# Kernel tuning notes

Measured on AMD Instinct MI355X. Metric: run time of the kernel, lower is better.

Reference implementation:

```python
import jax, jax.numpy as jnp
import numpy as np

BN_EPS = 1e-5


def setup_inputs() -> dict:
    key = jax.random.key(0)
    k1, k2, k3, k4, k5 = jax.random.split(key, 5)
    B, M, N = 4, 65536, 16384
    C_pre, C_cur, D_out = 64, 128, 128
    C_in = C_pre + C_cur  # 192
    pre_x = jax.random.normal(k1, (B, C_pre, M), dtype=jnp.float32)
    cur_x = jax.random.normal(k2, (B, C_cur, N), dtype=jnp.float32)
    up_idx = jax.random.randint(k3, (B, M, 1), 0, N, dtype=jnp.int64)
    w = jax.random.normal(k4, (C_in, D_out), dtype=jnp.float32) * 0.05
    b = jax.random.normal(k5, (D_out,), dtype=jnp.float32) * 0.05
    gamma = jnp.ones((D_out,), dtype=jnp.float32)
    beta = jnp.zeros((D_out,), dtype=jnp.float32)
    run_mean = jnp.zeros((D_out,), dtype=jnp.float32)
    run_var = jnp.ones((D_out,), dtype=jnp.float32)
    return {"pre_x": pre_x, "cur_x": cur_x, "up_idx": up_idx, "w": w, "b": b,
            "gamma": gamma, "beta": beta, "run_mean": run_mean, "run_var": run_var}


def reference(pre_x, cur_x, up_idx, w, b, gamma, beta, run_mean, run_var):
    # indexing_neighbor(cur_x.permute(0,2,1), up_idx).squeeze(2):
    # gather coarse-point features at nearest-neighbor indices -> [B, C_cur, M]
    idx = up_idx[:, :, 0]                                   # [B, M]
    feat = jnp.take_along_axis(cur_x, idx[:, None, :], axis=2)  # [B, C_cur, M]
    x = jnp.concatenate([pre_x, feat], axis=1)              # [B, C_in, M]
    # ConvTranspose1d(kernel=1) == pointwise linear with weight [C_in, D_out]
    y = jnp.einsum('bcm,cd->bdm', x, w) + b[None, :, None]  # [B, D_out, M]
    # BatchNorm1d (inference form with running stats) + ReLU
    inv = jax.lax.rsqrt(run_var + BN_EPS)
    y = (y - run_mean[None, :, None]) * (inv * gamma)[None, :, None] + beta[None, :, None]
    y = jnp.maximum(y, 0.0)
    return y.transpose(0, 2, 1)                             # [B, M, D_out]
```

## Files before the change

### kernel.cpp

```cpp
#include <hip/hip_runtime.h>
#include <hip/hip_bf16.h>


typedef short bhalf8 __attribute__((ext_vector_type(8)));
typedef float f32x4 __attribute__((ext_vector_type(4)));
typedef unsigned int u32x4 __attribute__((ext_vector_type(4)));

__device__ __forceinline__ short f2bf(float f) {
  unsigned int u = __float_as_uint(f);
  unsigned int r = (u + 0x7fffu + ((u >> 16) & 1u)) >> 16;
  return (short)r;
}

__global__ __launch_bounds__(256) void transpose_cur(const float* __restrict__ cur,
                                                     short* __restrict__ curT) {
  __shared__ float tile[128][65];
  const int b = blockIdx.y;
  const int n0 = blockIdx.x << 6;
  const float* src = cur + (size_t)b * 128 * 16384;
#pragma unroll
  for (int it = 0; it < 8; ++it) {
    int v = it * 256 + threadIdx.x;
    int cc = v >> 4;
    int nq = (v & 15) << 2;
    f32x4 f = __builtin_nontemporal_load(
        reinterpret_cast<const f32x4*>(&src[(size_t)cc * 16384 + n0 + nq]));
    tile[cc][nq + 0] = f[0];
    tile[cc][nq + 1] = f[1];
    tile[cc][nq + 2] = f[2];
    tile[cc][nq + 3] = f[3];
  }
  __syncthreads();
  short* dst = curT + ((size_t)b * 16384 + n0) * 128;
#pragma unroll
  for (int it = 0; it < 4; ++it) {
    int v = it * 256 + threadIdx.x;
    int nn = v >> 4;
    int c8 = (v & 15) << 3;
    bhalf8 pk;
#pragma unroll
    for (int j = 0; j < 8; ++j) pk[j] = f2bf(tile[c8 + j][nn]);
    *reinterpret_cast<bhalf8*>(&dst[(size_t)nn * 128 + c8]) = pk;
  }
}

#define NBLK 2048

__global__ __launch_bounds__(256, 3) void fused_gemm(
    const float* __restrict__ pre_x,
    const int* __restrict__ up_idx,
    const float* __restrict__ w,
    const float* __restrict__ bias,
    const float* __restrict__ gamma, const float* __restrict__ beta,
    const float* __restrict__ rmean, const float* __restrict__ rvar,
    const short* __restrict__ curT,
    float* __restrict__ out)
{
  __shared__ short x_lds[64 * 200];
  const int tid = threadIdx.x;
  const int lane = tid & 63;
  const int wv = tid >> 6;
  const int c = lane & 15;
  const int g = lane >> 4;

  bhalf8 bf[6][2];
#pragma unroll
  for (int s = 0; s < 6; ++s)
#pragma unroll
    for (int ct = 0; ct < 2; ++ct) {
      const int col = 32 * wv + 16 * ct + c;
#pragma unroll
      for (int j = 0; j < 8; ++j)
        bf[s][ct][j] = f2bf(w[(32 * s + 8 * g + j) * 128 + col]);
    }

  float scale[2], shift[2];
#pragma unroll
  for (int ct = 0; ct < 2; ++ct) {
    const int d = 32 * wv + 16 * ct + c;
    float sc = gamma[d] * rsqrtf(rvar[d] + 1e-5f);
    scale[ct] = sc;
    shift[ct] = (bias[d] - rmean[d]) * sc + beta[d];
  }

  for (int t = 0; t < 2; ++t) {
    const long rg = blockIdx.x + (long)t * NBLK;
    const long r0 = rg << 6;
    const int b = (int)(r0 >> 16);
    const int m0 = (int)(r0 & 65535);
    if (t) __syncthreads();

    {
      const float* pb = pre_x + (size_t)b * 64 * 65536 + m0;
#pragma unroll
      for (int it = 0; it < 4; ++it) {
        int v = it * 256 + tid;
        int cc = v >> 4;
        int mq = (v & 15) << 2;
        f32x4 f = __builtin_nontemporal_load(
            reinterpret_cast<const f32x4*>(&pb[(size_t)cc * 65536 + mq]));
        x_lds[(mq + 0) * 200 + cc] = f2bf(f[0]);
        x_lds[(mq + 1) * 200 + cc] = f2bf(f[1]);
        x_lds[(mq + 2) * 200 + cc] = f2bf(f[2]);
        x_lds[(mq + 3) * 200 + cc] = f2bf(f[3]);
      }
    }
    {
#pragma unroll
      for (int it = 0; it < 4; ++it) {
        int mm = it * 16 + (tid >> 4);
        int seg = tid & 15;
        int n = up_idx[r0 + mm];
        const short* srcp = curT + ((size_t)b * 16384 + n) * 128 + seg * 8;
        *reinterpret_cast<u32x4*>(&x_lds[mm * 200 + 64 + seg * 8]) =
            *reinterpret_cast<const u32x4*>(srcp);
      }
    }
    __syncthreads();

#pragma unroll
    for (int rt = 0; rt < 4; ++rt) {
      bhalf8 a[6];
#pragma unroll
      for (int s = 0; s < 6; ++s)
        a[s] = *reinterpret_cast<const bhalf8*>(
            &x_lds[(16 * rt + c) * 200 + 32 * s + 8 * g]);
      f32x4 acc0 = {0.f, 0.f, 0.f, 0.f};
      f32x4 acc1 = {0.f, 0.f, 0.f, 0.f};
#pragma unroll
      for (int s = 0; s < 6; ++s) {
        acc0 = __builtin_amdgcn_mfma_f32_16x16x32_bf16(a[s], bf[s][0], acc0, 0, 0, 0);
        acc1 = __builtin_amdgcn_mfma_f32_16x16x32_bf16(a[s], bf[s][1], acc1, 0, 0, 0);
      }
      float* ob = out + (size_t)(r0 + 16 * rt + 4 * g) * 128 + 32 * wv;
#pragma unroll
      for (int i = 0; i < 4; ++i) {
        float v0 = fmaxf(acc0[i] * scale[0] + shift[0], 0.f);
        float v1 = fmaxf(acc1[i] * scale[1] + shift[1], 0.f);
        __builtin_nontemporal_store(v0, ob + (size_t)i * 128 + c);
        __builtin_nontemporal_store(v1, ob + (size_t)i * 128 + 16 + c);
      }
    }
  }
}

extern "C" void kernel_launch(void* const* d_in, const int* in_sizes, int n_in,
                              void* d_out, int out_size, void* d_ws, size_t ws_size,
                              hipStream_t stream) {
  const float* pre_x = (const float*)d_in[0];
  const float* cur_x = (const float*)d_in[1];
  const int* up_idx = (const int*)d_in[2];
  const float* w = (const float*)d_in[3];
  const float* bias = (const float*)d_in[4];
  const float* gamma = (const float*)d_in[5];
  const float* beta = (const float*)d_in[6];
  const float* rmean = (const float*)d_in[7];
  const float* rvar = (const float*)d_in[8];
  float* out = (float*)d_out;
  short* curT = (short*)d_ws;

  hipLaunchKernelGGL(transpose_cur, dim3(256, 4), dim3(256), 0, stream, cur_x, curT);
  hipLaunchKernelGGL(fused_gemm, dim3(NBLK), dim3(256), 0, stream, pre_x, up_idx, w,
                     bias, gamma, beta, rmean, rvar, curT, out);
}
```

Before: 237.7 us.

## Precompute cur_x projection before gather to shrink main GEMM K

The cur_x half of the weight is now applied to the coarse points first (a GEMM over 16384 points per batch that writes bf16 projections Z), and the main kernel gathers projected rows from Z instead of raw features. This works because a gather commutes with a pointwise linear map. The main kernel's K dimension drops from 192 to 64, which cuts MFMA work, register use and LDS size, and occupancy is raised to 4. In exchange the projection is rounded to bf16 before the pre_x contribution is added, and the first kernel now does a small GEMM instead of only transposing.

```diff
diff --git a/kernel.cpp b/kernel.cpp
--- a/kernel.cpp
+++ b/kernel.cpp
@@ -11,69 +11,113 @@
   unsigned int r = (u + 0x7fffu + ((u >> 16) & 1u)) >> 16;
   return (short)r;
 }
-
-__global__ __launch_bounds__(256) void transpose_cur(const float* __restrict__ cur,
-                                                     short* __restrict__ curT) {
-  __shared__ float tile[128][65];
-  const int b = blockIdx.y;
-  const int n0 = blockIdx.x << 6;
-  const float* src = cur + (size_t)b * 128 * 16384;
-#pragma unroll
-  for (int it = 0; it < 8; ++it) {
-    int v = it * 256 + threadIdx.x;
-    int cc = v >> 4;
-    int nq = (v & 15) << 2;
-    f32x4 f = __builtin_nontemporal_load(
-        reinterpret_cast<const f32x4*>(&src[(size_t)cc * 16384 + n0 + nq]));
-    tile[cc][nq + 0] = f[0];
-    tile[cc][nq + 1] = f[1];
-    tile[cc][nq + 2] = f[2];
-    tile[cc][nq + 3] = f[3];
-  }
-  __syncthreads();
-  short* dst = curT + ((size_t)b * 16384 + n0) * 128;
-#pragma unroll
-  for (int it = 0; it < 4; ++it) {
-    int v = it * 256 + threadIdx.x;
-    int nn = v >> 4;
-    int c8 = (v & 15) << 3;
-    bhalf8 pk;
-#pragma unroll
-    for (int j = 0; j < 8; ++j) pk[j] = f2bf(tile[c8 + j][nn]);
-    *reinterpret_cast<bhalf8*>(&dst[(size_t)nn * 128 + c8]) = pk;
-  }
-}
-
-#define NBLK 2048
-
-__global__ __launch_bounds__(256, 3) void fused_gemm(
-    const float* __restrict__ pre_x,
-    const int* __restrict__ up_idx,
-    const float* __restrict__ w,
-    const float* __restrict__ bias,
-    const float* __restrict__ gamma, const float* __restrict__ beta,
-    const float* __restrict__ rmean, const float* __restrict__ rvar,
-    const short* __restrict__ curT,
-    float* __restrict__ out)
-{
-  __shared__ short x_lds[64 * 200];
+__device__ __forceinline__ float bf2f(short s) {
+  return __uint_as_float(((unsigned int)(unsigned short)s) << 16);
+}
+
+#define ZST 136
+#define PST 72
+
+__global__ __launch_bounds__(256, 4) void cur_gemm(const float* __restrict__ cur,
+                                                   const float* __restrict__ w,
+                                                   short* __restrict__ Z) {
+  __shared__ short lds[64 * ZST];
   const int tid = threadIdx.x;
   const int lane = tid & 63;
   const int wv = tid >> 6;
   const int c = lane & 15;
   const int g = lane >> 4;
-
-  bhalf8 bf[6][2];
-#pragma unroll
-  for (int s = 0; s < 6; ++s)
+  const int r0 = blockIdx.x << 6;
+  const int b = r0 >> 14;
+  const int n0 = r0 & 16383;
+  const float* src = cur + (size_t)b * 128 * 16384 + n0;
+
+  bhalf8 bw[4][2];
+#pragma unroll
+  for (int s = 0; s < 4; ++s)
 #pragma unroll
     for (int ct = 0; ct < 2; ++ct) {
       const int col = 32 * wv + 16 * ct + c;
 #pragma unroll
       for (int j = 0; j < 8; ++j)
-        bf[s][ct][j] = f2bf(w[(32 * s + 8 * g + j) * 128 + col]);
-    }
-
+        bw[s][ct][j] = f2bf(w[(64 + 32 * s + 8 * g + j) * 128 + col]);
+    }
+
+#pragma unroll
+  for (int it = 0; it < 8; ++it) {
+    int v = it * 256 + tid;
+    int cc = v >> 4;
+    int nq = (v & 15) << 2;
+    f32x4 f = __builtin_nontemporal_load(
+        reinterpret_cast<const f32x4*>(&src[(size_t)cc * 16384 + nq]));
+#pragma unroll
+    for (int k = 0; k < 4; ++k) lds[(nq + k) * ZST + cc] = f2bf(f[k]);
+  }
+  __syncthreads();
+
+  f32x4 acc[4][2];
+#pragma unroll
+  for (int rt = 0; rt < 4; ++rt) {
+    bhalf8 a[4];
+#pragma unroll
+    for (int s = 0; s < 4; ++s)
+      a[s] = *reinterpret_cast<const bhalf8*>(&lds[(16 * rt + c) * ZST + 32 * s + 8 * g]);
+    acc[rt][0] = (f32x4){0.f, 0.f, 0.f, 0.f};
+    acc[rt][1] = (f32x4){0.f, 0.f, 0.f, 0.f};
+#pragma unroll
+    for (int s = 0; s < 4; ++s) {
+      acc[rt][0] = __builtin_amdgcn_mfma_f32_16x16x32_bf16(a[s], bw[s][0], acc[rt][0], 0, 0, 0);
+      acc[rt][1] = __builtin_amdgcn_mfma_f32_16x16x32_bf16(a[s], bw[s][1], acc[rt][1], 0, 0, 0);
+    }
+  }
+  __syncthreads();
+#pragma unroll
+  for (int rt = 0; rt < 4; ++rt)
+#pragma unroll
+    for (int ct = 0; ct < 2; ++ct)
+#pragma unroll
+      for (int i = 0; i < 4; ++i)
+        lds[(16 * rt + 4 * g + i) * ZST + 32 * wv + 16 * ct + c] = f2bf(acc[rt][ct][i]);
+  __syncthreads();
+  short* dst = Z + (size_t)r0 * 128;
+  const int row = tid >> 2, q = tid & 3;
+#pragma unroll
+  for (int u = 0; u < 4; ++u) {
+    bhalf8 pk = *reinterpret_cast<const bhalf8*>(&lds[row * ZST + q * 32 + 8 * u]);
+    __builtin_nontemporal_store(pk, reinterpret_cast<bhalf8*>(&dst[(size_t)row * 128 + q * 32 + 8 * u]));
+  }
+}
+
+#define NBLK 2048
+
+__global__ __launch_bounds__(256, 4) void fused_main(
+    const float* __restrict__ pre_x,
+    const int* __restrict__ up_idx,
+    const float* __restrict__ w,
+    const float* __restrict__ bias, const float* __restrict__ gamma,
+    const float* __restrict__ beta, const float* __restrict__ rmean,
+    const float* __restrict__ rvar,
+    const short* __restrict__ Z,
+    float* __restrict__ out)
+{
+  __shared__ short pre_lds[64 * PST];
+  __shared__ short z_lds[64 * ZST];
+  const int tid = threadIdx.x;
+  const int lane = tid & 63;
+  const int wv = tid >> 6;
+  const int c = lane & 15;
+  const int g = lane >> 4;
+
+  bhalf8 bw[2][2];
+#pragma unroll
+  for (int s = 0; s < 2; ++s)
+#pragma unroll
+    for (int ct = 0; ct < 2; ++ct) {
+      const int col = 32 * wv + 16 * ct + c;
+#pragma unroll
+      for (int j = 0; j < 8; ++j)
+        bw[s][ct][j] = f2bf(w[(32 * s + 8 * g + j) * 128 + col]);
+    }
   float scale[2], shift[2];
 #pragma unroll
   for (int ct = 0; ct < 2; ++ct) {
@@ -99,10 +143,8 @@
         int mq = (v & 15) << 2;
         f32x4 f = __builtin_nontemporal_load(
             reinterpret_cast<const f32x4*>(&pb[(size_t)cc * 65536 + mq]));
-        x_lds[(mq + 0) * 200 + cc] = f2bf(f[0]);
-        x_lds[(mq + 1) * 200 + cc] = f2bf(f[1]);
-        x_lds[(mq + 2) * 200 + cc] = f2bf(f[2]);
-        x_lds[(mq + 3) * 200 + cc] = f2bf(f[3]);
+#pragma unroll
+        for (int k = 0; k < 4; ++k) pre_lds[(mq + k) * PST + cc] = f2bf(f[k]);
       }
     }
     {
@@ -111,8 +153,8 @@
         int mm = it * 16 + (tid >> 4);
         int seg = tid & 15;
         int n = up_idx[r0 + mm];
-        const short* srcp = curT + ((size_t)b * 16384 + n) * 128 + seg * 8;
-        *reinterpret_cast<u32x4*>(&x_lds[mm * 200 + 64 + seg * 8]) =
+        const short* srcp = Z + ((size_t)b * 16384 + n) * 128 + seg * 8;
+        *reinterpret_cast<u32x4*>(&z_lds[mm * ZST + seg * 8]) =
             *reinterpret_cast<const u32x4*>(srcp);
       }
     }
@@ -120,23 +162,26 @@
 
 #pragma unroll
     for (int rt = 0; rt < 4; ++rt) {
-      bhalf8 a[6];
-#pragma unroll
-      for (int s = 0; s < 6; ++s)
+      bhalf8 a[2];
+#pragma unroll
+      for (int s = 0; s < 2; ++s)
         a[s] = *reinterpret_cast<const bhalf8*>(
-            &x_lds[(16 * rt + c) * 200 + 32 * s + 8 * g]);
+            &pre_lds[(16 * rt + c) * PST + 32 * s + 8 * g]);
       f32x4 acc0 = {0.f, 0.f, 0.f, 0.f};
       f32x4 acc1 = {0.f, 0.f, 0.f, 0.f};
 #pragma unroll
-      for (int s = 0; s < 6; ++s) {
-        acc0 = __builtin_amdgcn_mfma_f32_16x16x32_bf16(a[s], bf[s][0], acc0, 0, 0, 0);
-        acc1 = __builtin_amdgcn_mfma_f32_16x16x32_bf16(a[s], bf[s][1], acc1, 0, 0, 0);
+      for (int s = 0; s < 2; ++s) {
+        acc0 = __builtin_amdgcn_mfma_f32_16x16x32_bf16(a[s], bw[s][0], acc0, 0, 0, 0);
+        acc1 = __builtin_amdgcn_mfma_f32_16x16x32_bf16(a[s], bw[s][1], acc1, 0, 0, 0);
       }
       float* ob = out + (size_t)(r0 + 16 * rt + 4 * g) * 128 + 32 * wv;
 #pragma unroll
       for (int i = 0; i < 4; ++i) {
-        float v0 = fmaxf(acc0[i] * scale[0] + shift[0], 0.f);
-        float v1 = fmaxf(acc1[i] * scale[1] + shift[1], 0.f);
+        const short* zr = &z_lds[(16 * rt + 4 * g + i) * ZST + 32 * wv];
+        float z0 = bf2f(zr[c]);
+        float z1 = bf2f(zr[16 + c]);
+        float v0 = fmaxf((acc0[i] + z0) * scale[0] + shift[0], 0.f);
+        float v1 = fmaxf((acc1[i] + z1) * scale[1] + shift[1], 0.f);
         __builtin_nontemporal_store(v0, ob + (size_t)i * 128 + c);
         __builtin_nontemporal_store(v1, ob + (size_t)i * 128 + 16 + c);
       }
@@ -157,9 +202,9 @@
   const float* rmean = (const float*)d_in[7];
   const float* rvar = (const float*)d_in[8];
   float* out = (float*)d_out;
-  short* curT = (short*)d_ws;
-
-  hipLaunchKernelGGL(transpose_cur, dim3(256, 4), dim3(256), 0, stream, cur_x, curT);
-  hipLaunchKernelGGL(fused_gemm, dim3(NBLK), dim3(256), 0, stream, pre_x, up_idx, w,
-                     bias, gamma, beta, rmean, rvar, curT, out);
-}
+  short* Z = (short*)d_ws;
+
+  hipLaunchKernelGGL(cur_gemm, dim3(1024), dim3(256), 0, stream, cur_x, w, Z);
+  hipLaunchKernelGGL(fused_main, dim3(NBLK), dim3(256), 0, stream, pre_x, up_idx, w,
+                     bias, gamma, beta, rmean, rvar, Z, out);
+}
```

After: 248.2 us. 1.04x slower.
